# Optimization experiments

Hardware: AMD Instinct MI355X
Metric: run time of the kernel (lower is better)

## Reference

```python
import jax, jax.numpy as jnp
import numpy as np

# skimage uniform LBP (P=8, R=1) sample offsets: rr = -R*sin(2*pi*p/P), cc = R*cos(2*pi*p/P),
# rounded to 5 decimals as in skimage, with bilinear interpolation and cval=0 outside the image.
_P = 8
_OFFS = [(round(float(-np.sin(2.0 * np.pi * p / _P)), 5), round(float(np.cos(2.0 * np.pi * p / _P)), 5)) for p in range(_P)]


def _uniform_lbp(gray):
    """gray: [B, F, H, W] quantized float (0..255). Returns normalized uniform LBP, same shape."""
    B, F, H, W = gray.shape
    pad = jnp.pad(gray, ((0, 0), (0, 0), (1, 1), (1, 1)))  # zeros outside, matching skimage cval=0

    def shift(dr, dc):  # integer shift via slicing of the padded frame stack
        return pad[:, :, 1 + dr:1 + dr + H, 1 + dc:1 + dc + W]

    def sample(dr, dc):  # bilinear interpolation at fractional offset (dr, dc)
        r0, c0 = int(np.floor(dr)), int(np.floor(dc))
        fr, fc = dr - r0, dc - c0
        if fr < 1e-7 and fc < 1e-7:
            return shift(r0, c0)
        return ((1.0 - fr) * (1.0 - fc)) * shift(r0, c0) \
             + ((1.0 - fr) * fc) * shift(r0, c0 + 1) \
             + (fr * (1.0 - fc)) * shift(r0 + 1, c0) \
             + (fr * fc) * shift(r0 + 1, c0 + 1)

    bits = [(sample(dr, dc) >= gray) for (dr, dc) in _OFFS]
    ones = jnp.zeros(gray.shape, jnp.float32)
    changes = jnp.zeros(gray.shape, jnp.int32)
    for p in range(_P):
        ones = ones + bits[p].astype(jnp.float32)
        changes = changes + (bits[p] ^ bits[(p + 1) % _P]).astype(jnp.int32)
    lbp = jnp.where(changes <= 2, ones, jnp.float32(_P + 1))  # 'uniform' method: codes 0..9
    # per-frame normalization: lbp /= lbp.max() when max > 0
    m = lbp.max(axis=(2, 3), keepdims=True)
    return jnp.where(m > 0, lbp / jnp.maximum(m, 1.0), lbp)


def _conv3d(x, w, b, stride):
    y = jax.lax.conv_general_dilated(
        x, w, window_strides=stride, padding=[(1, 1)] * 3,
        dimension_numbers=("NCDHW", "OIDHW", "NCDHW"))
    return y + b[None, :, None, None, None]


def _enhanced_3d_cnn(lbp3, w1, b1, w2, b2):
    h = jax.nn.relu(_conv3d(lbp3, w1, b1, (1, 2, 2)))   # [B,64,F,H/2,W/2]
    h = jax.nn.relu(_conv3d(h, w2, b2, (2, 2, 2)))      # [B,128,F/2,H/4,W/4]
    return h.mean(axis=(2, 3, 4))                        # [B,128] global avg pool


def setup_inputs() -> dict:
    key = jax.random.key(0)
    k1, k2, k3 = jax.random.split(key, 3)
    x = jax.random.uniform(k1, (4, 3, 16, 224, 224), jnp.float32)
    w1 = jax.random.normal(k2, (64, 3, 3, 3, 3), jnp.float32) * 0.05
    b1 = jnp.zeros((64,), jnp.float32)
    w2 = jax.random.normal(k3, (128, 64, 3, 3, 3), jnp.float32) * 0.05
    b2 = jnp.zeros((128,), jnp.float32)
    return {"x": x, "w1": w1, "b1": b1, "w2": w2, "b2": b2}


def reference(x, w1, b1, w2, b2):
    B, C, F, H, W = x.shape
    gray = jnp.floor(x.mean(axis=1) * 255.0)         # == (gray*255).astype(uint8) for x in [0,1]
    lbp = _uniform_lbp(gray)                          # [B,F,H,W]
    lbp3 = jnp.broadcast_to(lbp[:, None], (B, 3, F, H, W))
    return _enhanced_3d_cnn(lbp3, w1, b1, w2, b2)     # [B,128]
```

## Files before the change

kernel.cpp:

```cpp
#include <hip/hip_runtime.h>
#include <hip/hip_bf16.h>
#include <stdint.h>

constexpr int NB = 4;
constexpr int NF = 16;
constexpr int NH = 224, NW = 224;
constexpr int HWPIX = NH * NW;
constexpr int NPIX = NB * NF * HWPIX;
constexpr int OC2 = 128;

typedef __attribute__((ext_vector_type(8))) __bf16 bf16x8;
typedef __attribute__((ext_vector_type(4))) float f32x4;

#define MFMA16(a, b, c) __builtin_amdgcn_mfma_f32_16x16x32_bf16(a, b, c, 0, 0, 0)

__device__ __forceinline__ ushort bf16u(float f) {
  __hip_bfloat16 h = __float2bfloat16(f);
  return *(ushort*)&h;
}

__global__ __launch_bounds__(256) void graylbp_kernel(const float* __restrict__ x,
                                                      unsigned char* __restrict__ lbpc,
                                                      int* __restrict__ blockmax) {
  __shared__ float sg[18 * 18];
  const int tile = blockIdx.x;
  const int frame = blockIdx.y;
  const int ty = tile / 14, tx = tile - ty * 14;
  const int b = frame >> 4, f = frame & 15;
  const float* xb = x + ((size_t)b * 3 * NF + f) * HWPIX;

  for (int e = threadIdx.x; e < 324; e += 256) {
    int r = e / 18, cc = e - 18 * r;
    int y = ty * 16 + r - 1, xx = tx * 16 + cc - 1;
    float v = 0.0f;
    if ((unsigned)y < (unsigned)NH && (unsigned)xx < (unsigned)NW) {
      size_t o = (size_t)y * NW + xx;
      float s = xb[o] + xb[o + (size_t)NF * HWPIX] + xb[o + 2 * (size_t)NF * HWPIX];
      v = floorf((s / 3.0f) * 255.0f);
    }
    sg[e] = v;
  }
  __syncthreads();

  const int r = threadIdx.x >> 4, cc = threadIdx.x & 15;
  float n[3][3];
#pragma unroll
  for (int dy = 0; dy < 3; ++dy)
#pragma unroll
    for (int dx = 0; dx < 3; ++dx) n[dy][dx] = sg[(r + dy) * 18 + (cc + dx)];
  float c = n[1][1];

  constexpr double Ad = 0.70711;
  constexpr double Bd = 1.0 - Ad;

  const float s0 = n[1][2];
  const float s2 = n[0][1];
  const float s4 = n[1][0];
  const float s6 = n[2][1];
  const float s1 = (float)(Ad * Bd) * n[0][1] + (float)(Ad * Ad) * n[0][2]
                 + (float)(Bd * Bd) * n[1][1] + (float)(Bd * Ad) * n[1][2];
  const float s3 = (float)(Ad * Ad) * n[0][0] + (float)(Ad * Bd) * n[0][1]
                 + (float)(Bd * Ad) * n[1][0] + (float)(Bd * Bd) * n[1][1];
  const float s5 = (float)(Bd * Ad) * n[1][0] + (float)(Bd * Bd) * n[1][1]
                 + (float)(Ad * Ad) * n[2][0] + (float)(Ad * Bd) * n[2][1];
  const float s7 = (float)(Bd * Bd) * n[1][1] + (float)(Bd * Ad) * n[1][2]
                 + (float)(Ad * Bd) * n[2][1] + (float)(Ad * Ad) * n[2][2];

  bool bb[8] = { s0 >= c, s1 >= c, s2 >= c, s3 >= c,
                 s4 >= c, s5 >= c, s6 >= c, s7 >= c };
  int ones = 0, changes = 0;
#pragma unroll
  for (int p = 0; p < 8; ++p) {
    ones += bb[p] ? 1 : 0;
    changes += (bb[p] != bb[(p + 1) & 7]) ? 1 : 0;
  }
  int code = (changes <= 2) ? ones : 9;
  lbpc[(size_t)frame * HWPIX + (ty * 16 + r) * NW + tx * 16 + cc] = (unsigned char)code;

  int m = code;
#pragma unroll
  for (int off = 32; off >= 1; off >>= 1) m = max(m, __shfl_down(m, off, 64));
  __shared__ int wm[4];
  if ((threadIdx.x & 63) == 0) wm[threadIdx.x >> 6] = m;
  __syncthreads();
  if (threadIdx.x == 0)
    blockmax[frame * 196 + tile] = max(max(wm[0], wm[1]), max(wm[2], wm[3]));
}

__global__ void framemax_tab_kernel(const int* __restrict__ blockmax,
                                    __hip_bfloat16* __restrict__ normtab) {
  int t = threadIdx.x;
  int f = t >> 2, part = t & 3;
  int m = 0;
  for (int j = part; j < 196; j += 4) m = max(m, blockmax[f * 196 + j]);
  m = max(m, __shfl_xor(m, 1, 64));
  m = max(m, __shfl_xor(m, 2, 64));
  if (part == 0) {
    for (int cde = 0; cde < 16; ++cde) {
      float v = (m > 0) ? ((float)cde / (float)m) : (float)cde;
      normtab[f * 16 + cde] = __float2bfloat16(v);
    }
  }
}

__global__ __launch_bounds__(256) void normlbp_kernel(const unsigned char* __restrict__ lbpc,
                                                      const __hip_bfloat16* __restrict__ normtab,
                                                      __hip_bfloat16* __restrict__ lbpn) {
  int i = blockIdx.x * 256 + threadIdx.x;
  int frame = (i * 8) / HWPIX;
  const ushort* tab = (const ushort*)normtab + frame * 16;
  uint2 cds = *(const uint2*)(lbpc + (size_t)i * 8);
  uint o0 = (uint)tab[cds.x & 0xFF] | ((uint)tab[(cds.x >> 8) & 0xFF] << 16);
  uint o1 = (uint)tab[(cds.x >> 16) & 0xFF] | ((uint)tab[cds.x >> 24] << 16);
  uint o2 = (uint)tab[cds.y & 0xFF] | ((uint)tab[(cds.y >> 8) & 0xFF] << 16);
  uint o3 = (uint)tab[(cds.y >> 16) & 0xFF] | ((uint)tab[cds.y >> 24] << 16);
  uint4 ov; ov.x = o0; ov.y = o1; ov.z = o2; ov.w = o3;
  *(uint4*)((ushort*)lbpn + (size_t)i * 8) = ov;
}

__global__ void w1m_kernel(const float* __restrict__ w1, const float* __restrict__ b1,
                           __hip_bfloat16* __restrict__ w1m1,
                           __hip_bfloat16* __restrict__ w1m2) {
  int o = threadIdx.x;
  if (o >= 64) return;
  float wsum[27];
  for (int t = 0; t < 27; ++t)
    wsum[t] = w1[o * 81 + t] + w1[o * 81 + 27 + t] + w1[o * 81 + 54 + t];
  for (int k = 0; k < 32; ++k) {
    int r = k >> 2, el = k & 3;
    float v1 = 0.0f, v2 = 0.0f;
    if (r < 3 && el >= 1) v1 = wsum[r * 3 + el - 1];
    if (r == 3 && el == 0) v1 = b1[o];
    if (r >= 4 && r < 7 && el >= 1) v1 = wsum[9 + (r - 4) * 3 + el - 1];
    if (r < 3 && el >= 1) v2 = wsum[18 + r * 3 + el - 1];
    w1m1[o * 32 + k] = __float2bfloat16(v1);
    w1m2[o * 32 + k] = __float2bfloat16(v2);
  }
}

__global__ __launch_bounds__(256) void w2r_kernel(const float* __restrict__ w2,
                                                  __hip_bfloat16* __restrict__ w2r) {
  int i = blockIdx.x * 256 + threadIdx.x;
  if (i >= 27 * 128 * 64) return;
  int tap = i / (128 * 64);
  int rem = i - tap * (128 * 64);
  int oc = rem >> 6, ic = rem & 63;
  w2r[i] = __float2bfloat16(w2[((size_t)oc * 64 + ic) * 27 + tap]);
}

constexpr int ROWB2 = 57 * 256;

__global__ __launch_bounds__(256, 2) void fused_conv(
    const __hip_bfloat16* __restrict__ lbpn,
    const __hip_bfloat16* __restrict__ w1m1,
    const __hip_bfloat16* __restrict__ w1m2,
    const __hip_bfloat16* __restrict__ w2r,
    const float* __restrict__ b2,
    float* __restrict__ partial) {
  __shared__ __align__(16) char slab[5 * ROWB2];

  const int wg = blockIdx.x;
  const int swz = (wg & 7) * 112 + (wg >> 3);
  const int gg = swz % 28;
  const int rem = swz / 28;
  const int f2 = rem & 7;
  const int b = rem >> 3;

  const int tid = threadIdx.x;
  const int lane = tid & 63, w = tid >> 6;
  const int c = lane & 15, q = lane >> 4;
  const int oc0 = w * 32;
  const f32x4 zero4 = {0.f, 0.f, 0.f, 0.f};

  int x2v[7], rb2[7];
#pragma unroll
  for (int j = 0; j < 7; ++j) {
    int pos = j * 16 + c;
    int yo = pos >= 56 ? 1 : 0;
    x2v[j] = pos - 56 * yo;
    rb2[j] = yo * 2 * ROWB2 + x2v[j] * 256;
  }

  bf16x8 am1[4], am2[4];
  const __bf16* w1m1b = (const __bf16*)w1m1;
  const __bf16* w1m2b = (const __bf16*)w1m2;
#pragma unroll
  for (int ocg = 0; ocg < 4; ++ocg) {
    am1[ocg] = *(const bf16x8*)(w1m1b + ((ocg * 16 + c) << 5) + q * 8);
    am2[ocg] = *(const bf16x8*)(w1m2b + ((ocg * 16 + c) << 5) + q * 8);
  }

  const int rid0 = 2 * q - (q >> 1);
  const int rid1 = rid0 + 1;
  const bool use1 = (q == 0) || (q == 2);
  const int rid2 = (q == 0) ? 6 : 8;
  const bool use2 = (q <= 1);
  const bool use3 = (q == 0);
  const bool biasl = (q == 1);

  float bias[2][4];
#pragma unroll
  for (int i = 0; i < 2; ++i)
#pragma unroll
    for (int r = 0; r < 4; ++r) bias[i][r] = b2[oc0 + i * 16 + q * 4 + r];

  f32x4 acc[2][7];
#pragma unroll
  for (int i = 0; i < 2; ++i)
#pragma unroll
    for (int j = 0; j < 7; ++j) acc[i][j] = zero4;

  const __bf16* w2rb = (const __bf16*)w2r;
  const char* lbpnb = (const char*)lbpn;

  if (tid < 40) {
    int r = tid >> 3, u = tid & 7;
    *(int4*)(slab + r * ROWB2 + (u >> 2) * 128 + (u & 3) * 16) = make_int4(0, 0, 0, 0);
  }

  auto rowld = [&](int f1, int rid, bool use, int y1, long xb, uint& lo, uint& hi) {
    int kfc = (rid >= 6) ? 2 : (rid >= 3 ? 1 : 0);
    int ky = rid - kfc * 3;
    int fin = f1 - 1 + kfc;
    int yin = 2 * y1 - 1 + ky;
    bool ok = use && ((unsigned)fin < (unsigned)NF) && ((unsigned)yin < (unsigned)NH);
    long off = ok ? (((long)(b * NF + fin) * HWPIX + (long)yin * NW) * 2 + xb) : 0;
    uint l = *(const uint*)(lbpnb + off);
    uint h = *(const uint*)(lbpnb + off + 4);
    lo = ok ? l : 0u;
    hi = ok ? h : 0u;
  };

  auto CONV1 = [&](int kf) {
    const int f1 = 2 * f2 - 1 + kf;
    if ((unsigned)f1 >= (unsigned)NF) return;
    for (int fi = w; fi < 35; fi += 4) {
      int rr = fi / 7, fx = fi - 7 * rr;
      int y1 = 4 * gg - 1 + rr;
      int xs = fx * 16 + c + 1;
      int t = xs >> 1, k7 = t & 7, sub = xs & 1;
      char* wbase = slab + rr * ROWB2 + t * 256 + (q & 1) * 8;
      if ((unsigned)y1 < 112u) {
        const int x1 = fx * 16 + c;
        const long xb = (long)(4 * x1 - 4);
        uint r0l, r0h, r1l, r1h, r2l, r2h, r3l, r3h;
        rowld(f1, rid0, true, y1, xb, r0l, r0h);
        rowld(f1, rid1, use1, y1, xb, r1l, r1h);
        rowld(f1, rid2, use2, y1, xb, r2l, r2h);
        rowld(f1, 7,    use3, y1, xb, r3l, r3h);
        if (x1 == 0) {
          r0l &= 0xFFFFu; r1l &= 0xFFFFu; r2l &= 0xFFFFu; r3l &= 0xFFFFu;
        }
        if (biasl) { r1l = 0x3F80u; r1h = 0u; }
        union U8 { bf16x8 v; uint u[4]; } b1u, b2u;
        b1u.u[0] = r0l; b1u.u[1] = r0h; b1u.u[2] = r1l; b1u.u[3] = r1h;
        b2u.u[0] = r2l; b2u.u[1] = r2h; b2u.u[2] = r3l; b2u.u[3] = r3h;
#pragma unroll
        for (int ocg = 0; ocg < 4; ++ocg) {
          f32x4 a = MFMA16(am1[ocg], b1u.v, zero4);
          a = MFMA16(am2[ocg], b2u.v, a);
          ushort4 o;
          o.x = bf16u(fmaxf(a[0], 0.0f));
          o.y = bf16u(fmaxf(a[1], 0.0f));
          o.z = bf16u(fmaxf(a[2], 0.0f));
          o.w = bf16u(fmaxf(a[3], 0.0f));
          int ich = ocg >> 1;
          int g8 = sub * 4 + (ocg & 1) * 2 + (q >> 1);
          *(ushort4*)(wbase + ich * 128 + ((g8 ^ k7) << 4)) = o;
        }
      } else {
        ushort4 z; z.x = z.y = z.z = z.w = 0;
#pragma unroll
        for (int ocg = 0; ocg < 4; ++ocg) {
          int ich = ocg >> 1;
          int g8 = sub * 4 + (ocg & 1) * 2 + (q >> 1);
          *(ushort4*)(wbase + ich * 128 + ((g8 ^ k7) << 4)) = z;
        }
      }
    }
  };

  CONV1(0);

  for (int kf = 0; kf < 3; ++kf) {
    __syncthreads();
    const int f1 = 2 * f2 - 1 + kf;
    const bool fok = (unsigned)f1 < (unsigned)NF;

    if (fok) {
#pragma unroll
      for (int ky = 0; ky < 3; ++ky) {
#pragma unroll
        for (int kx = 0; kx < 3; ++kx) {
          const int tap = kf * 9 + ky * 3 + kx;
          const int sx = kx >> 1;
          const int sb4 = (kx & 1) * 4 + q;
          const int immr = ky * ROWB2 + sx * 256;
#pragma unroll
          for (int ich = 0; ich < 2; ++ich) {
            const __bf16* wtap = w2rb + (((size_t)tap * 128 + oc0 + c) << 6)
                               + ich * 32 + q * 8;
            bf16x8 a0 = *(const bf16x8*)(wtap);
            bf16x8 a1 = *(const bf16x8*)(wtap + (16 << 6));
#pragma unroll
            for (int j = 0; j < 7; ++j) {
              int slot = sb4 ^ ((x2v[j] + sx) & 7);
              bf16x8 bv = *(const bf16x8*)(slab + rb2[j] + immr + ich * 128 + (slot << 4));
              acc[0][j] = MFMA16(a0, bv, acc[0][j]);
              acc[1][j] = MFMA16(a1, bv, acc[1][j]);
            }
          }
        }
      }
    }

    __syncthreads();
    if (kf < 2) CONV1(kf + 1);
  }

#pragma unroll
  for (int i = 0; i < 2; ++i) {
#pragma unroll
    for (int r = 0; r < 4; ++r) {
      float s = 0.0f;
#pragma unroll
      for (int j = 0; j < 7; ++j) s += fmaxf(acc[i][j][r] + bias[i][r], 0.0f);
      s += __shfl_xor(s, 1);
      s += __shfl_xor(s, 2);
      s += __shfl_xor(s, 4);
      s += __shfl_xor(s, 8);
      if (c == 0) {
        int oc = oc0 + i * 16 + q * 4 + r;
        partial[((size_t)b * OC2 + oc) * 224 + f2 * 28 + gg] = s;
      }
    }
  }
}

__global__ void final_kernel(const float* __restrict__ partial, float* __restrict__ out) {
  int i = blockIdx.x * 256 + threadIdx.x;
  float s = 0.0f;
  for (int j = 0; j < 224; ++j) s += partial[(size_t)i * 224 + j];
  out[i] = s / 25088.0f;
}

extern "C" void kernel_launch(void* const* d_in, const int* in_sizes, int n_in,
                              void* d_out, int out_size, void* d_ws, size_t ws_size,
                              hipStream_t stream) {
  const float* x  = (const float*)d_in[0];
  const float* w1 = (const float*)d_in[1];
  const float* b1 = (const float*)d_in[2];
  const float* w2 = (const float*)d_in[3];
  const float* b2 = (const float*)d_in[4];
  float* out = (float*)d_out;

  char* ws = (char*)d_ws;
  unsigned char* lbpc = (unsigned char*)ws;
  int* blockmax = (int*)(ws + 3211264);
  __hip_bfloat16* normtab = (__hip_bfloat16*)(ws + 3261440);
  float* partial = (float*)(ws + 3263488);
  __hip_bfloat16* w2r = (__hip_bfloat16*)(ws + 3722240);
  __hip_bfloat16* w1m1 = (__hip_bfloat16*)(ws + 4164608);
  __hip_bfloat16* w1m2 = (__hip_bfloat16*)(ws + 4168704);
  __hip_bfloat16* lbpn = (__hip_bfloat16*)(ws + 4172800);

  w1m_kernel<<<1, 64, 0, stream>>>(w1, b1, w1m1, w1m2);
  w2r_kernel<<<(27 * 128 * 64 + 255) / 256, 256, 0, stream>>>(w2, w2r);
  graylbp_kernel<<<dim3(196, NB * NF), 256, 0, stream>>>(x, lbpc, blockmax);
  framemax_tab_kernel<<<1, 256, 0, stream>>>(blockmax, normtab);
  normlbp_kernel<<<NPIX / 8 / 256, 256, 0, stream>>>(lbpc, normtab, lbpn);
  fused_conv<<<896, 256, 0, stream>>>(lbpn, w1m1, w1m2, w2r, b2, partial);
  final_kernel<<<2, 256, 0, stream>>>(partial, out);
}
```

Before: 135.4 us.

## Split fused conv tiles in half along x to double workgroups and occupancy

Each fused conv workgroup now covers half the output width (28 conv2 columns plus a halo) rather than the full 56, so the grid doubles to 1792 workgroups and the LDS slab roughly halves. This allows launch bounds of 4 waves per SIMD and per-thread accumulators drop from 7 to 4 column groups. The cost is redundant conv1 recomputation on the halo columns, a partially wasted MFMA column group (masked in the reduction), and a final reduction over twice as many partial sums.

```diff
diff --git a/kernel.cpp b/kernel.cpp
--- a/kernel.cpp
+++ b/kernel.cpp
@@ -148,23 +148,25 @@
   w2r[i] = __float2bfloat16(w2[((size_t)oc * 64 + ic) * 27 + tap]);
 }
 
-constexpr int ROWB2 = 57 * 256;
-
-__global__ __launch_bounds__(256, 2) void fused_conv(
+constexpr int ROWX = 29 * 256;
+
+__global__ __launch_bounds__(256, 4) void fused_conv(
     const __hip_bfloat16* __restrict__ lbpn,
     const __hip_bfloat16* __restrict__ w1m1,
     const __hip_bfloat16* __restrict__ w1m2,
     const __hip_bfloat16* __restrict__ w2r,
     const float* __restrict__ b2,
     float* __restrict__ partial) {
-  __shared__ __align__(16) char slab[5 * ROWB2];
+  __shared__ __align__(16) char slab[5 * ROWX];
 
   const int wg = blockIdx.x;
-  const int swz = (wg & 7) * 112 + (wg >> 3);
+  const int swz = (wg & 7) * 224 + (wg >> 3);
   const int gg = swz % 28;
-  const int rem = swz / 28;
-  const int f2 = rem & 7;
-  const int b = rem >> 3;
+  const int u = swz / 28;
+  const int xh = u & 1;
+  const int f2 = (u >> 1) & 7;
+  const int b = u >> 4;
+  const int key4 = 4 * xh;
 
   const int tid = threadIdx.x;
   const int lane = tid & 63, w = tid >> 6;
@@ -172,14 +174,17 @@
   const int oc0 = w * 32;
   const f32x4 zero4 = {0.f, 0.f, 0.f, 0.f};
 
-  int x2v[7], rb2[7];
-#pragma unroll
-  for (int j = 0; j < 7; ++j) {
+  int x2v[4], rb2[4]; bool pv3;
+#pragma unroll
+  for (int j = 0; j < 4; ++j) {
     int pos = j * 16 + c;
-    int yo = pos >= 56 ? 1 : 0;
-    x2v[j] = pos - 56 * yo;
-    rb2[j] = yo * 2 * ROWB2 + x2v[j] * 256;
-  }
+    int yo = pos >= 28 ? 1 : 0;
+    int x2l = pos - 28 * yo;
+    if (pos >= 56) { x2l = 27; yo = 1; }
+    x2v[j] = x2l;
+    rb2[j] = yo * 2 * ROWX + x2l * 256;
+  }
+  pv3 = (c < 8);
 
   bf16x8 am1[4], am2[4];
   const __bf16* w1m1b = (const __bf16*)w1m1;
@@ -204,19 +209,14 @@
 #pragma unroll
     for (int r = 0; r < 4; ++r) bias[i][r] = b2[oc0 + i * 16 + q * 4 + r];
 
-  f32x4 acc[2][7];
+  f32x4 acc[2][4];
 #pragma unroll
   for (int i = 0; i < 2; ++i)
 #pragma unroll
-    for (int j = 0; j < 7; ++j) acc[i][j] = zero4;
+    for (int j = 0; j < 4; ++j) acc[i][j] = zero4;
 
   const __bf16* w2rb = (const __bf16*)w2r;
   const char* lbpnb = (const char*)lbpn;
-
-  if (tid < 40) {
-    int r = tid >> 3, u = tid & 7;
-    *(int4*)(slab + r * ROWB2 + (u >> 2) * 128 + (u & 3) * 16) = make_int4(0, 0, 0, 0);
-  }
 
   auto rowld = [&](int f1, int rid, bool use, int y1, long xb, uint& lo, uint& hi) {
     int kfc = (rid >= 6) ? 2 : (rid >= 3 ? 1 : 0);
@@ -234,14 +234,15 @@
   auto CONV1 = [&](int kf) {
     const int f1 = 2 * f2 - 1 + kf;
     if ((unsigned)f1 >= (unsigned)NF) return;
-    for (int fi = w; fi < 35; fi += 4) {
-      int rr = fi / 7, fx = fi - 7 * rr;
-      int y1 = 4 * gg - 1 + rr;
-      int xs = fx * 16 + c + 1;
-      int t = xs >> 1, k7 = t & 7, sub = xs & 1;
-      char* wbase = slab + rr * ROWB2 + t * 256 + (q & 1) * 8;
-      if ((unsigned)y1 < 112u) {
-        const int x1 = fx * 16 + c;
+    for (int fi = w; fi < 20; fi += 4) {
+      const int fx = fi / 5, rr = fi - 5 * fx;
+      const int xs_l = fx * 16 + c;
+      if (xs_l >= 58) continue;
+      const int y1 = 4 * gg - 1 + rr;
+      const int x1 = 56 * xh + xs_l - 1;
+      const int t = xs_l >> 1, k7 = (t + key4) & 7, sub = xs_l & 1;
+      char* wbase = slab + rr * ROWX + t * 256 + (q & 1) * 8;
+      if ((unsigned)y1 < 112u && (unsigned)x1 < 112u) {
         const long xb = (long)(4 * x1 - 4);
         uint r0l, r0h, r1l, r1h, r2l, r2h, r3l, r3h;
         rowld(f1, rid0, true, y1, xb, r0l, r0h);
@@ -295,7 +296,7 @@
           const int tap = kf * 9 + ky * 3 + kx;
           const int sx = kx >> 1;
           const int sb4 = (kx & 1) * 4 + q;
-          const int immr = ky * ROWB2 + sx * 256;
+          const int immr = ky * ROWX + sx * 256;
 #pragma unroll
           for (int ich = 0; ich < 2; ++ich) {
             const __bf16* wtap = w2rb + (((size_t)tap * 128 + oc0 + c) << 6)
@@ -303,8 +304,8 @@
             bf16x8 a0 = *(const bf16x8*)(wtap);
             bf16x8 a1 = *(const bf16x8*)(wtap + (16 << 6));
 #pragma unroll
-            for (int j = 0; j < 7; ++j) {
-              int slot = sb4 ^ ((x2v[j] + sx) & 7);
+            for (int j = 0; j < 4; ++j) {
+              int slot = sb4 ^ ((x2v[j] + sx + key4) & 7);
               bf16x8 bv = *(const bf16x8*)(slab + rb2[j] + immr + ich * 128 + (slot << 4));
               acc[0][j] = MFMA16(a0, bv, acc[0][j]);
               acc[1][j] = MFMA16(a1, bv, acc[1][j]);
@@ -324,14 +325,15 @@
     for (int r = 0; r < 4; ++r) {
       float s = 0.0f;
 #pragma unroll
-      for (int j = 0; j < 7; ++j) s += fmaxf(acc[i][j][r] + bias[i][r], 0.0f);
+      for (int j = 0; j < 3; ++j) s += fmaxf(acc[i][j][r] + bias[i][r], 0.0f);
+      if (pv3) s += fmaxf(acc[i][3][r] + bias[i][r], 0.0f);
       s += __shfl_xor(s, 1);
       s += __shfl_xor(s, 2);
       s += __shfl_xor(s, 4);
       s += __shfl_xor(s, 8);
       if (c == 0) {
         int oc = oc0 + i * 16 + q * 4 + r;
-        partial[((size_t)b * OC2 + oc) * 224 + f2 * 28 + gg] = s;
+        partial[((size_t)b * OC2 + oc) * 448 + (f2 * 28 + gg) * 2 + xh] = s;
       }
     }
   }
@@ -340,7 +342,7 @@
 __global__ void final_kernel(const float* __restrict__ partial, float* __restrict__ out) {
   int i = blockIdx.x * 256 + threadIdx.x;
   float s = 0.0f;
-  for (int j = 0; j < 224; ++j) s += partial[(size_t)i * 224 + j];
+  for (int j = 0; j < 448; ++j) s += partial[(size_t)i * 448 + j];
   out[i] = s / 25088.0f;
 }
 
@@ -359,16 +361,16 @@
   int* blockmax = (int*)(ws + 3211264);
   __hip_bfloat16* normtab = (__hip_bfloat16*)(ws + 3261440);
   float* partial = (float*)(ws + 3263488);
-  __hip_bfloat16* w2r = (__hip_bfloat16*)(ws + 3722240);
-  __hip_bfloat16* w1m1 = (__hip_bfloat16*)(ws + 4164608);
-  __hip_bfloat16* w1m2 = (__hip_bfloat16*)(ws + 4168704);
-  __hip_bfloat16* lbpn = (__hip_bfloat16*)(ws + 4172800);
+  __hip_bfloat16* w2r = (__hip_bfloat16*)(ws + 4180992);
+  __hip_bfloat16* w1m1 = (__hip_bfloat16*)(ws + 4623360);
+  __hip_bfloat16* w1m2 = (__hip_bfloat16*)(ws + 4627456);
+  __hip_bfloat16* lbpn = (__hip_bfloat16*)(ws + 4631552);
 
   w1m_kernel<<<1, 64, 0, stream>>>(w1, b1, w1m1, w1m2);
   w2r_kernel<<<(27 * 128 * 64 + 255) / 256, 256, 0, stream>>>(w2, w2r);
   graylbp_kernel<<<dim3(196, NB * NF), 256, 0, stream>>>(x, lbpc, blockmax);
   framemax_tab_kernel<<<1, 256, 0, stream>>>(blockmax, normtab);
   normlbp_kernel<<<NPIX / 8 / 256, 256, 0, stream>>>(lbpc, normtab, lbpn);
-  fused_conv<<<896, 256, 0, stream>>>(lbpn, w1m1, w1m2, w2r, b2, partial);
+  fused_conv<<<1792, 256, 0, stream>>>(lbpn, w1m1, w1m2, w2r, b2, partial);
   final_kernel<<<2, 256, 0, stream>>>(partial, out);
 }
```

Measured after the change: 179.5 us. 32.5% more time.

## Prefetch next frame's conv1 input rows into registers during conv2 MFMA loop

Applied to the files above, without the earlier changes.

Splits the fused conv1 stage into a global-load phase and a compute/store phase. Loads for the next input frame are issued before the conv2 MFMA loop on the current slab, so their latency overlaps the matrix work, and the conv1 MFMAs and LDS stores run after the barrier. This holds 72 extra registers per thread, which may raise register pressure, cause spills or lower occupancy.

```diff
diff --git a/kernel.cpp b/kernel.cpp
--- a/kernel.cpp
+++ b/kernel.cpp
@@ -231,61 +231,88 @@
     hi = ok ? h : 0u;
   };
 
-  auto CONV1 = [&](int kf) {
+  uint L[9][8];
+
+  auto C1LOAD = [&](int kf) {
     const int f1 = 2 * f2 - 1 + kf;
     if ((unsigned)f1 >= (unsigned)NF) return;
-    for (int fi = w; fi < 35; fi += 4) {
-      int rr = fi / 7, fx = fi - 7 * rr;
-      int y1 = 4 * gg - 1 + rr;
-      int xs = fx * 16 + c + 1;
-      int t = xs >> 1, k7 = t & 7, sub = xs & 1;
-      char* wbase = slab + rr * ROWB2 + t * 256 + (q & 1) * 8;
-      if ((unsigned)y1 < 112u) {
+#pragma unroll
+    for (int it = 0; it < 9; ++it) {
+      const int fi = w + 4 * it;
+      if (fi < 35) {
+        const int rr = fi / 7, fx = fi - 7 * rr;
+        const int y1 = 4 * gg - 1 + rr;
         const int x1 = fx * 16 + c;
+        const bool dok = (unsigned)y1 < 112u;
         const long xb = (long)(4 * x1 - 4);
-        uint r0l, r0h, r1l, r1h, r2l, r2h, r3l, r3h;
-        rowld(f1, rid0, true, y1, xb, r0l, r0h);
-        rowld(f1, rid1, use1, y1, xb, r1l, r1h);
-        rowld(f1, rid2, use2, y1, xb, r2l, r2h);
-        rowld(f1, 7,    use3, y1, xb, r3l, r3h);
-        if (x1 == 0) {
-          r0l &= 0xFFFFu; r1l &= 0xFFFFu; r2l &= 0xFFFFu; r3l &= 0xFFFFu;
-        }
-        if (biasl) { r1l = 0x3F80u; r1h = 0u; }
-        union U8 { bf16x8 v; uint u[4]; } b1u, b2u;
-        b1u.u[0] = r0l; b1u.u[1] = r0h; b1u.u[2] = r1l; b1u.u[3] = r1h;
-        b2u.u[0] = r2l; b2u.u[1] = r2h; b2u.u[2] = r3l; b2u.u[3] = r3h;
-#pragma unroll
-        for (int ocg = 0; ocg < 4; ++ocg) {
-          f32x4 a = MFMA16(am1[ocg], b1u.v, zero4);
-          a = MFMA16(am2[ocg], b2u.v, a);
-          ushort4 o;
-          o.x = bf16u(fmaxf(a[0], 0.0f));
-          o.y = bf16u(fmaxf(a[1], 0.0f));
-          o.z = bf16u(fmaxf(a[2], 0.0f));
-          o.w = bf16u(fmaxf(a[3], 0.0f));
-          int ich = ocg >> 1;
-          int g8 = sub * 4 + (ocg & 1) * 2 + (q >> 1);
-          *(ushort4*)(wbase + ich * 128 + ((g8 ^ k7) << 4)) = o;
-        }
-      } else {
-        ushort4 z; z.x = z.y = z.z = z.w = 0;
-#pragma unroll
-        for (int ocg = 0; ocg < 4; ++ocg) {
-          int ich = ocg >> 1;
-          int g8 = sub * 4 + (ocg & 1) * 2 + (q >> 1);
-          *(ushort4*)(wbase + ich * 128 + ((g8 ^ k7) << 4)) = z;
+        rowld(f1, rid0, dok, y1, xb, L[it][0], L[it][1]);
+        rowld(f1, rid1, dok && use1, y1, xb, L[it][2], L[it][3]);
+        rowld(f1, rid2, dok && use2, y1, xb, L[it][4], L[it][5]);
+        rowld(f1, 7,    dok && use3, y1, xb, L[it][6], L[it][7]);
+      }
+    }
+  };
+
+  auto C1STORE = [&](int kf) {
+    const int f1 = 2 * f2 - 1 + kf;
+    if ((unsigned)f1 >= (unsigned)NF) return;
+#pragma unroll
+    for (int it = 0; it < 9; ++it) {
+      const int fi = w + 4 * it;
+      if (fi < 35) {
+        const int rr = fi / 7, fx = fi - 7 * rr;
+        const int y1 = 4 * gg - 1 + rr;
+        const int xs = fx * 16 + c + 1;
+        const int t = xs >> 1, k7 = t & 7, sub = xs & 1;
+        char* wbase = slab + rr * ROWB2 + t * 256 + (q & 1) * 8;
+        if ((unsigned)y1 < 112u) {
+          const int x1 = fx * 16 + c;
+          uint r0l = L[it][0], r0h = L[it][1];
+          uint r1l = L[it][2], r1h = L[it][3];
+          uint r2l = L[it][4], r2h = L[it][5];
+          uint r3l = L[it][6], r3h = L[it][7];
+          if (x1 == 0) {
+            r0l &= 0xFFFFu; r1l &= 0xFFFFu; r2l &= 0xFFFFu; r3l &= 0xFFFFu;
+          }
+          if (biasl) { r1l = 0x3F80u; r1h = 0u; }
+          union U8 { bf16x8 v; uint u[4]; } b1u, b2u;
+          b1u.u[0] = r0l; b1u.u[1] = r0h; b1u.u[2] = r1l; b1u.u[3] = r1h;
+          b2u.u[0] = r2l; b2u.u[1] = r2h; b2u.u[2] = r3l; b2u.u[3] = r3h;
+#pragma unroll
+          for (int ocg = 0; ocg < 4; ++ocg) {
+            f32x4 a = MFMA16(am1[ocg], b1u.v, zero4);
+            a = MFMA16(am2[ocg], b2u.v, a);
+            ushort4 o;
+            o.x = bf16u(fmaxf(a[0], 0.0f));
+            o.y = bf16u(fmaxf(a[1], 0.0f));
+            o.z = bf16u(fmaxf(a[2], 0.0f));
+            o.w = bf16u(fmaxf(a[3], 0.0f));
+            int ich = ocg >> 1;
+            int g8 = sub * 4 + (ocg & 1) * 2 + (q >> 1);
+            *(ushort4*)(wbase + ich * 128 + ((g8 ^ k7) << 4)) = o;
+          }
+        } else {
+          ushort4 z; z.x = z.y = z.z = z.w = 0;
+#pragma unroll
+          for (int ocg = 0; ocg < 4; ++ocg) {
+            int ich = ocg >> 1;
+            int g8 = sub * 4 + (ocg & 1) * 2 + (q >> 1);
+            *(ushort4*)(wbase + ich * 128 + ((g8 ^ k7) << 4)) = z;
+          }
         }
       }
     }
   };
 
-  CONV1(0);
+  C1LOAD(0);
+  C1STORE(0);
 
   for (int kf = 0; kf < 3; ++kf) {
     __syncthreads();
     const int f1 = 2 * f2 - 1 + kf;
     const bool fok = (unsigned)f1 < (unsigned)NF;
+
+    if (kf < 2) C1LOAD(kf + 1);
 
     if (fok) {
 #pragma unroll
@@ -315,7 +342,7 @@
     }
 
     __syncthreads();
-    if (kf < 2) CONV1(kf + 1);
+    if (kf < 2) C1STORE(kf + 1);
   }
 
 #pragma unroll
```

After: 232.3 us. 71.6% more time.
